# Kernel optimization log

Hardware: AMD Instinct MI355X
Metric: run time of the kernel (lower is better)

## Reference

```python
import jax, jax.numpy as jnp
import numpy as np

EMB = 1024
HEADS = 16
HEAD_DIM = EMB // HEADS  # 64


def setup_inputs() -> dict:
    key = jax.random.key(0)
    ks = jax.random.split(key, 11)
    B, S = 2, 2048
    scale = 1.0 / np.sqrt(EMB)
    inp = {
        "xv": jax.random.normal(ks[0], (B, S, EMB), jnp.float32),
        "xk": jax.random.normal(ks[1], (B, S, EMB), jnp.float32),
        "xq": jax.random.normal(ks[2], (B, S, EMB), jnp.float32),
        "Wq": jax.random.normal(ks[3], (EMB, EMB), jnp.float32) * scale,
        "bq": jax.random.normal(ks[4], (EMB,), jnp.float32) * 0.01,
        "Wk": jax.random.normal(ks[5], (EMB, EMB), jnp.float32) * scale,
        "bk": jax.random.normal(ks[6], (EMB,), jnp.float32) * 0.01,
        "Wv": jax.random.normal(ks[7], (EMB, EMB), jnp.float32) * scale,
        "bv": jax.random.normal(ks[8], (EMB,), jnp.float32) * 0.01,
        "Wo": jax.random.normal(ks[9], (EMB, EMB), jnp.float32) * scale,
        "bo": jax.random.normal(ks[10], (EMB,), jnp.float32) * 0.01,
    }
    return inp


def reference(xv, xk, xq, Wq, bq, Wk, bk, Wv, bv, Wo, bo):
    B, S, E = xq.shape
    H, D = HEADS, HEAD_DIM
    # projections (x @ W + b), split into heads: [B,S,H,D]
    Q = (xq @ Wq + bq).reshape(B, S, H, D)
    K = (xk @ Wk + bk).reshape(B, S, H, D)
    V = (xv @ Wv + bv).reshape(B, S, H, D)
    # scaled dot-product attention per head (vectorized over heads)
    scores = jnp.einsum("bqhd,bkhd->bhqk", Q, K) / jnp.sqrt(jnp.float32(D))
    attn = jax.nn.softmax(scores, axis=-1)
    ctx = jnp.einsum("bhqk,bkhd->bqhd", attn, V).reshape(B, S, E)
    return ctx @ Wo + bo
```

## Files before the change

### kernel.cpp

```cpp
#include <hip/hip_runtime.h>
#include <hip/hip_bf16.h>

typedef __hip_bfloat16 bf16;
typedef __attribute__((ext_vector_type(8))) short short8;
typedef __attribute__((ext_vector_type(4))) short short4v;
typedef __attribute__((ext_vector_type(4))) float floatx4;

#define MFMA16 __builtin_amdgcn_mfma_f32_16x16x32_bf16
#define BARRIER __builtin_amdgcn_s_barrier
#define SCHEDB0() __builtin_amdgcn_sched_barrier(0)
#define SETPRIO __builtin_amdgcn_s_setprio


__device__ __forceinline__ void gl16(const void* g, void* l) {
    __builtin_amdgcn_global_load_lds(
        (const __attribute__((address_space(1))) void*)g,
        (__attribute__((address_space(3))) void*)l, 16, 0, 0);
}

__global__ __launch_bounds__(256) void wtrans_k(const float* __restrict__ w0,
                                                const float* __restrict__ w1,
                                                const float* __restrict__ w2,
                                                const float* __restrict__ w3,
                                                bf16* __restrict__ dst) {
    const float* srcs[4] = {w0, w1, w2, w3};
    const float* src = srcs[blockIdx.z];
    bf16* d = dst + (size_t)blockIdx.z * 1024 * 1024;
    __shared__ float t[32][33];
    int tx = threadIdx.x, ty = threadIdx.y;
    int x0 = blockIdx.x * 32, y0 = blockIdx.y * 32;
#pragma unroll
    for (int i = 0; i < 4; i++)
        t[ty + i * 8][tx] = src[(size_t)(y0 + ty + i * 8) * 1024 + x0 + tx];
    __syncthreads();
#pragma unroll
    for (int i = 0; i < 4; i++)
        d[(size_t)(x0 + ty + i * 8) * 1024 + y0 + tx] =
            __float2bfloat16(t[tx][ty + i * 8]);
}

__global__ __launch_bounds__(256) void xcast_k(const float* __restrict__ x0,
                                               const float* __restrict__ x1,
                                               const float* __restrict__ x2,
                                               bf16* __restrict__ dst) {
    const float* srcs[3] = {x0, x1, x2};
    const float* src = srcs[blockIdx.y];
    bf16* d = dst + (size_t)blockIdx.y * (4096 * 1024);
    size_t i = (size_t)blockIdx.x * 256 + threadIdx.x;
    const float4* s4 = (const float4*)src + i * 2;
    float4 a = s4[0], b = s4[1];
    union { __hip_bfloat162 h2[4]; short8 s; } pk;
    pk.h2[0] = __float22bfloat162_rn(make_float2(a.x, a.y));
    pk.h2[1] = __float22bfloat162_rn(make_float2(a.z, a.w));
    pk.h2[2] = __float22bfloat162_rn(make_float2(b.x, b.y));
    pk.h2[3] = __float22bfloat162_rn(make_float2(b.z, b.w));
    *(short8*)&d[i * 8] = pk.s;
}

__global__ __launch_bounds__(256) void qkv_k(const bf16* __restrict__ xb,
                                             const bf16* __restrict__ wt,
                                             const float* __restrict__ bq,
                                             const float* __restrict__ bk,
                                             const float* __restrict__ bv,
                                             bf16* __restrict__ Qw,
                                             bf16* __restrict__ Kw,
                                             bf16* __restrict__ Vt) {
    __shared__ __align__(16) bf16 lA[3][128 * 32];
    __shared__ __align__(16) bf16 lB[3][128 * 32];
    int z = blockIdx.z;
    const bf16* A = xb + (size_t)z * (4096 * 1024);
    const bf16* Bt = wt + (size_t)z * (1024 * 1024);
    const float* bias = (z == 0) ? bq : (z == 1) ? bk : bv;
    int m0 = blockIdx.x * 128, n0 = blockIdx.y * 128;
    int tid = threadIdx.x, wave = tid >> 6, lane = tid & 63;
    int lm = lane & 15, quad = lane >> 4;
    int wm = wave >> 1, wn = wave & 1;
    int swb = quad ^ ((lm >> 1) & 3);

    floatx4 acc[4][4];
#pragma unroll
    for (int i = 0; i < 4; i++)
#pragma unroll
        for (int j = 0; j < 4; j++) acc[i][j] = (floatx4){0.f, 0.f, 0.f, 0.f};

    auto stage = [&](int bufi, int kt) {
#pragma unroll
        for (int q2 = 0; q2 < 2; q2++) {
            int slot0 = wave * 128 + q2 * 64;
            int r = (slot0 + lane) >> 2;
            int c = (lane & 3) ^ ((r >> 1) & 3);
            gl16(&A[(size_t)(m0 + r) * 1024 + kt * 32 + c * 8],
                 &lA[bufi][slot0 * 8]);
            gl16(&Bt[(size_t)(n0 + r) * 1024 + kt * 32 + c * 8],
                 &lB[bufi][slot0 * 8]);
        }
    };

    auto compute = [&](int cur) {
        short8 af[4], bfr[4];
#pragma unroll
        for (int ms = 0; ms < 4; ms++) {
            int r = wm * 64 + ms * 16 + lm;
            af[ms] = *(const short8*)&lA[cur][(r * 4 + swb) * 8];
        }
#pragma unroll
        for (int ns = 0; ns < 4; ns++) {
            int r = wn * 64 + ns * 16 + lm;
            bfr[ns] = *(const short8*)&lB[cur][(r * 4 + swb) * 8];
        }
        SETPRIO(1);
#pragma unroll
        for (int ms = 0; ms < 4; ms++)
#pragma unroll
            for (int ns = 0; ns < 4; ns++)
                acc[ms][ns] = MFMA16(af[ms], bfr[ns], acc[ms][ns], 0, 0, 0);
        SETPRIO(0);
    };

    stage(0, 0);
    stage(1, 1);
    for (int kt = 0; kt < 32; kt++) {
        int cur = kt % 3;
        BARRIER();
        if (kt < 30) {
            stage((kt + 2) % 3, kt + 2);
            asm volatile("s_waitcnt vmcnt(8)" ::: "memory");
        } else if (kt == 30) {
            asm volatile("s_waitcnt vmcnt(4)" ::: "memory");
        } else {
            asm volatile("s_waitcnt vmcnt(0)" ::: "memory");
        }
        BARRIER();
        SCHEDB0();
        compute(cur);
    }

    bf16* dstQK = (z == 0) ? Qw : Kw;
    float scale = (z == 0) ? 0.125f * 1.44269504f : 1.0f;
#pragma unroll
    for (int ms = 0; ms < 4; ms++) {
        int rowb = m0 + wm * 64 + ms * 16 + quad * 4;
        int bb = rowb >> 11, s0 = rowb & 2047;
#pragma unroll
        for (int ns = 0; ns < 4; ns++) {
            int col = n0 + wn * 64 + ns * 16 + lm;
            float bvv = bias[col];
            int hh = col >> 6, d = col & 63;
            if (z < 2) {
#pragma unroll
                for (int rr = 0; rr < 4; rr++) {
                    float v = (acc[ms][ns][rr] + bvv) * scale;
                    dstQK[((((size_t)bb * 16 + hh) * 2048 + s0 + rr) << 6) + d] =
                        __float2bfloat16(v);
                }
            } else {
                short4v pk;
#pragma unroll
                for (int rr = 0; rr < 4; rr++) {
                    bf16 h = __float2bfloat16(acc[ms][ns][rr] + bvv);
                    pk[rr] = *(short*)&h;
                }
                *(short4v*)&Vt[((((size_t)bb * 16 + hh) * 64 + d) << 11) + s0] = pk;
            }
        }
    }
}

__global__ __launch_bounds__(256) void outproj_k(const bf16* __restrict__ ctx,
                                                 const bf16* __restrict__ wot,
                                                 const float* __restrict__ bo,
                                                 float* __restrict__ out) {
    __shared__ __align__(16) bf16 lA[2][128 * 32];
    __shared__ __align__(16) bf16 lB[2][64 * 32];
    int m0 = blockIdx.x * 128, n0 = blockIdx.y * 64;
    int tid = threadIdx.x, wave = tid >> 6, lane = tid & 63;
    int lm = lane & 15, quad = lane >> 4;
    int wm = wave >> 1, wn = wave & 1;
    int swb = quad ^ ((lm >> 1) & 3);

    floatx4 acc[4][2];
#pragma unroll
    for (int i = 0; i < 4; i++)
#pragma unroll
        for (int j = 0; j < 2; j++) acc[i][j] = (floatx4){0.f, 0.f, 0.f, 0.f};

    auto stage = [&](int bufi, int kt) {
#pragma unroll
        for (int q2 = 0; q2 < 2; q2++) {
            int slot0 = wave * 128 + q2 * 64;
            int r = (slot0 + lane) >> 2;
            int c = (lane & 3) ^ ((r >> 1) & 3);
            gl16(&ctx[(size_t)(m0 + r) * 1024 + kt * 32 + c * 8],
                 &lA[bufi][slot0 * 8]);
        }
        {
            int slot0 = wave * 64;
            int r = (slot0 + lane) >> 2;
            int c = (lane & 3) ^ ((r >> 1) & 3);
            gl16(&wot[(size_t)(n0 + r) * 1024 + kt * 32 + c * 8],
                 &lB[bufi][slot0 * 8]);
        }
    };

    auto compute = [&](int cur) {
        short8 af[4], bfr[2];
#pragma unroll
        for (int ms = 0; ms < 4; ms++) {
            int r = wm * 64 + ms * 16 + lm;
            af[ms] = *(const short8*)&lA[cur][(r * 4 + swb) * 8];
        }
#pragma unroll
        for (int ns = 0; ns < 2; ns++) {
            int r = wn * 32 + ns * 16 + lm;
            bfr[ns] = *(const short8*)&lB[cur][(r * 4 + swb) * 8];
        }
        SETPRIO(1);
#pragma unroll
        for (int ms = 0; ms < 4; ms++)
#pragma unroll
            for (int ns = 0; ns < 2; ns++)
                acc[ms][ns] = MFMA16(af[ms], bfr[ns], acc[ms][ns], 0, 0, 0);
        SETPRIO(0);
    };

    stage(0, 0);
    for (int kt = 0; kt < 31; kt++) {
        int cur = kt & 1;
        BARRIER();
        stage(cur ^ 1, kt + 1);
        asm volatile("s_waitcnt vmcnt(3)" ::: "memory");
        BARRIER();
        SCHEDB0();
        compute(cur);
    }
    BARRIER();
    asm volatile("s_waitcnt vmcnt(0)" ::: "memory");
    BARRIER();
    SCHEDB0();
    compute(1);

#pragma unroll
    for (int ms = 0; ms < 4; ms++) {
        int rowb = m0 + wm * 64 + ms * 16 + quad * 4;
#pragma unroll
        for (int ns = 0; ns < 2; ns++) {
            int col = n0 + wn * 32 + ns * 16 + lm;
            float bvv = bo[col];
#pragma unroll
            for (int rr = 0; rr < 4; rr++)
                out[(size_t)(rowb + rr) * 1024 + col] = acc[ms][ns][rr] + bvv;
        }
    }
}

__global__ __launch_bounds__(512, 4) void attn_k(const bf16* __restrict__ Q,
                                                 const bf16* __restrict__ K,
                                                 const bf16* __restrict__ Vt,
                                                 bf16* __restrict__ ctx) {
    __shared__ __align__(16) bf16 lKV[2][2][64 * 64];
    __shared__ float scrL[4][32];
    int bh = blockIdx.x, qt = blockIdx.y;
    int b = bh >> 4, h = bh & 15;
    const bf16* Qh = Q + (size_t)bh * (2048 * 64);
    const bf16* Kh = K + (size_t)bh * (2048 * 64);
    const bf16* Vh = Vt + (size_t)bh * (64 * 2048);
    int tid = threadIdx.x, wave = tid >> 6, lane = tid & 63;
    int lm = lane & 15, quad = lane >> 4;
    int s7 = lm & 7;
    int wq = wave >> 1, wk = wave & 1;

    short8 qf[2][2];
#pragma unroll
    for (int qblk = 0; qblk < 2; qblk++) {
        int qrow = qt * 128 + wq * 32 + qblk * 16 + lm;
        qf[qblk][0] = *(const short8*)&Qh[(size_t)qrow * 64 + quad * 8];
        qf[qblk][1] = *(const short8*)&Qh[(size_t)qrow * 64 + 32 + quad * 8];
    }

    short8 onesf;
#pragma unroll
    for (int i = 0; i < 8; i++) onesf[i] = (short)0x3F80;

    floatx4 o[2][4];
#pragma unroll
    for (int i = 0; i < 2; i++)
#pragma unroll
        for (int j = 0; j < 4; j++) o[i][j] = (floatx4){0.f, 0.f, 0.f, 0.f};
    floatx4 accL[2];
#pragma unroll
    for (int i = 0; i < 2; i++) accL[i] = (floatx4){0.f, 0.f, 0.f, 0.f};

    auto stage = [&](int bufi, int kt) {
        int slot0 = wave * 64;
        int r = (slot0 + lane) >> 3;
        int c = (lane & 7) ^ (r & 7);
        gl16(&Kh[(size_t)(kt * 64 + r) * 64 + c * 8], &lKV[0][bufi][slot0 * 8]);
        gl16(&Vh[(size_t)r * 2048 + kt * 64 + c * 8], &lKV[1][bufi][slot0 * 8]);
    };

    auto compute = [&](int cur) {
        short8 kf[2][2];
#pragma unroll
        for (int ksub = 0; ksub < 2; ksub++) {
            int r = wk * 32 + ksub * 16 + lm;
#pragma unroll
            for (int ds = 0; ds < 2; ds++)
                kf[ksub][ds] = *(const short8*)
                    &lKV[0][cur][(r * 8 + ((ds * 4 + quad) ^ s7)) * 8];
        }
        floatx4 s[2][2];
#pragma unroll
        for (int i = 0; i < 2; i++)
#pragma unroll
            for (int j = 0; j < 2; j++) s[i][j] = (floatx4){0.f, 0.f, 0.f, 0.f};
        SETPRIO(1);
#pragma unroll
        for (int qblk = 0; qblk < 2; qblk++)
#pragma unroll
            for (int ksub = 0; ksub < 2; ksub++) {
                s[qblk][ksub] = MFMA16(kf[ksub][0], qf[qblk][0], s[qblk][ksub], 0, 0, 0);
                s[qblk][ksub] = MFMA16(kf[ksub][1], qf[qblk][1], s[qblk][ksub], 0, 0, 0);
            }
        SETPRIO(0);

        short8 pz[2];
#pragma unroll
        for (int qblk = 0; qblk < 2; qblk++) {
            union { short4v h[2]; short8 s8; } up;
#pragma unroll
            for (int ksub = 0; ksub < 2; ksub++) {
                float p0 = __builtin_amdgcn_exp2f(s[qblk][ksub][0]);
                float p1 = __builtin_amdgcn_exp2f(s[qblk][ksub][1]);
                float p2 = __builtin_amdgcn_exp2f(s[qblk][ksub][2]);
                float p3 = __builtin_amdgcn_exp2f(s[qblk][ksub][3]);
                union { __hip_bfloat162 b2[2]; short4v s4; } c;
                c.b2[0] = __float22bfloat162_rn(make_float2(p0, p1));
                c.b2[1] = __float22bfloat162_rn(make_float2(p2, p3));
                up.h[ksub] = c.s4;
            }
            pz[qblk] = up.s8;
        }

        short8 vfz[4];
#pragma unroll
        for (int dblk = 0; dblk < 4; dblk++) {
            int d = dblk * 16 + lm;
            union { short4v h[2]; short8 s8; } uv;
#pragma unroll
            for (int ksub = 0; ksub < 2; ksub++) {
                int g = 4 * wk + 2 * ksub + (quad >> 1);
                uv.h[ksub] = *(const short4v*)
                    &lKV[1][cur][(d * 8 + (g ^ s7)) * 8 + (quad & 1) * 4];
            }
            vfz[dblk] = uv.s8;
        }

        SETPRIO(1);
#pragma unroll
        for (int qblk = 0; qblk < 2; qblk++) {
            accL[qblk] = MFMA16(pz[qblk], onesf, accL[qblk], 0, 0, 0);
#pragma unroll
            for (int dblk = 0; dblk < 4; dblk++)
                o[qblk][dblk] = MFMA16(pz[qblk], vfz[dblk], o[qblk][dblk], 0, 0, 0);
        }
        SETPRIO(0);
    };

    stage(0, 0);
    for (int kt = 0; kt < 31; kt++) {
        int cur = kt & 1;
        BARRIER();
        stage(cur ^ 1, kt + 1);
        asm volatile("s_waitcnt vmcnt(2)" ::: "memory");
        BARRIER();
        SCHEDB0();
        compute(cur);
    }
    BARRIER();
    asm volatile("s_waitcnt vmcnt(0)" ::: "memory");
    BARRIER();
    SCHEDB0();
    compute(1);

    __syncthreads();
    float* scrO = (float*)&lKV[0][0][0];
    if (wk == 1) {
#pragma unroll
        for (int qblk = 0; qblk < 2; qblk++) {
#pragma unroll
            for (int dblk = 0; dblk < 4; dblk++)
#pragma unroll
                for (int rr = 0; rr < 4; rr++)
                    scrO[wq * 2048 + (qblk * 16 + quad * 4 + rr) * 64 +
                         dblk * 16 + lm] = o[qblk][dblk][rr];
#pragma unroll
            for (int rr = 0; rr < 4; rr++)
                scrL[wq][qblk * 16 + quad * 4 + rr] = accL[qblk][rr];
        }
    }
    __syncthreads();
    if (wk == 0) {
#pragma unroll
        for (int qblk = 0; qblk < 2; qblk++) {
            float inv[4];
#pragma unroll
            for (int rr = 0; rr < 4; rr++)
                inv[rr] = 1.f / (accL[qblk][rr] +
                                 scrL[wq][qblk * 16 + quad * 4 + rr]);
#pragma unroll
            for (int dblk = 0; dblk < 4; dblk++) {
                int e = h * 64 + dblk * 16 + lm;
#pragma unroll
                for (int rr = 0; rr < 4; rr++) {
                    int srow = qt * 128 + wq * 32 + qblk * 16 + quad * 4 + rr;
                    float of = o[qblk][dblk][rr] +
                               scrO[wq * 2048 + (qblk * 16 + quad * 4 + rr) * 64 +
                                    dblk * 16 + lm];
                    ctx[(size_t)(b * 2048 + srow) * 1024 + e] =
                        __float2bfloat16(of * inv[rr]);
                }
            }
        }
    }
}

extern "C" void kernel_launch(void* const* d_in, const int* in_sizes, int n_in,
                              void* d_out, int out_size, void* d_ws, size_t ws_size,
                              hipStream_t stream) {
    const float* xv = (const float*)d_in[0];
    const float* xk = (const float*)d_in[1];
    const float* xq = (const float*)d_in[2];
    const float* Wq = (const float*)d_in[3];
    const float* bq = (const float*)d_in[4];
    const float* Wk = (const float*)d_in[5];
    const float* bk = (const float*)d_in[6];
    const float* Wv = (const float*)d_in[7];
    const float* bv = (const float*)d_in[8];
    const float* Wo = (const float*)d_in[9];
    const float* bo = (const float*)d_in[10];
    float* out = (float*)d_out;
    bf16* ws = (bf16*)d_ws;

    const size_t MB1 = 1024 * 1024;
    bf16* wt  = ws;
    bf16* Qw  = ws + 4 * MB1;
    bf16* Kw  = ws + 8 * MB1;
    bf16* Vt  = ws + 12 * MB1;
    bf16* ctx = ws + 16 * MB1;
    bf16* xb  = ws + 20 * MB1;

    hipLaunchKernelGGL(wtrans_k, dim3(32, 32, 4), dim3(32, 8), 0, stream,
                       Wq, Wk, Wv, Wo, wt);

    hipLaunchKernelGGL(xcast_k, dim3(2048, 3), dim3(256), 0, stream,
                       xq, xk, xv, xb);

    hipLaunchKernelGGL(qkv_k, dim3(32, 8, 3), dim3(256), 0, stream,
                       xb, wt, bq, bk, bv, Qw, Kw, Vt);

    hipLaunchKernelGGL(attn_k, dim3(32, 16), dim3(512), 0, stream, Qw, Kw, Vt, ctx);

    hipLaunchKernelGGL(outproj_k, dim3(32, 16), dim3(256), 0, stream,
                       ctx, wt + 3 * MB1, bo, out);
}
```

Before: 208.9 us.

## Double attention KV tile to 128 keys and merge prep kernels into one launch

The attention kernel now stages 128 keys per iteration instead of 64 into separate K and V LDS buffers. This halves the loop trip count and the barrier/wait overhead per key, and doubles the MFMA work between syncs. It costs more LDS per block (64KB total), which may cut occupancy below the launch_bounds target of 4 blocks. Separately, the weight-transpose and input-cast kernels are merged into one launch to save a kernel launch and its tail.

```diff
diff --git a/kernel.cpp b/kernel.cpp
--- a/kernel.cpp
+++ b/kernel.cpp
@@ -18,43 +18,48 @@
         (__attribute__((address_space(3))) void*)l, 16, 0, 0);
 }
 
-__global__ __launch_bounds__(256) void wtrans_k(const float* __restrict__ w0,
-                                                const float* __restrict__ w1,
-                                                const float* __restrict__ w2,
-                                                const float* __restrict__ w3,
-                                                bf16* __restrict__ dst) {
-    const float* srcs[4] = {w0, w1, w2, w3};
-    const float* src = srcs[blockIdx.z];
-    bf16* d = dst + (size_t)blockIdx.z * 1024 * 1024;
-    __shared__ float t[32][33];
-    int tx = threadIdx.x, ty = threadIdx.y;
-    int x0 = blockIdx.x * 32, y0 = blockIdx.y * 32;
-#pragma unroll
-    for (int i = 0; i < 4; i++)
-        t[ty + i * 8][tx] = src[(size_t)(y0 + ty + i * 8) * 1024 + x0 + tx];
-    __syncthreads();
-#pragma unroll
-    for (int i = 0; i < 4; i++)
-        d[(size_t)(x0 + ty + i * 8) * 1024 + y0 + tx] =
-            __float2bfloat16(t[tx][ty + i * 8]);
-}
-
-__global__ __launch_bounds__(256) void xcast_k(const float* __restrict__ x0,
-                                               const float* __restrict__ x1,
-                                               const float* __restrict__ x2,
-                                               bf16* __restrict__ dst) {
-    const float* srcs[3] = {x0, x1, x2};
-    const float* src = srcs[blockIdx.y];
-    bf16* d = dst + (size_t)blockIdx.y * (4096 * 1024);
-    size_t i = (size_t)blockIdx.x * 256 + threadIdx.x;
-    const float4* s4 = (const float4*)src + i * 2;
-    float4 a = s4[0], b = s4[1];
-    union { __hip_bfloat162 h2[4]; short8 s; } pk;
-    pk.h2[0] = __float22bfloat162_rn(make_float2(a.x, a.y));
-    pk.h2[1] = __float22bfloat162_rn(make_float2(a.z, a.w));
-    pk.h2[2] = __float22bfloat162_rn(make_float2(b.x, b.y));
-    pk.h2[3] = __float22bfloat162_rn(make_float2(b.z, b.w));
-    *(short8*)&d[i * 8] = pk.s;
+__global__ __launch_bounds__(256) void prep_k(const float* __restrict__ w0,
+                                              const float* __restrict__ w1,
+                                              const float* __restrict__ w2,
+                                              const float* __restrict__ w3,
+                                              bf16* __restrict__ wdst,
+                                              const float* __restrict__ x0,
+                                              const float* __restrict__ x1,
+                                              const float* __restrict__ x2,
+                                              bf16* __restrict__ xdst) {
+    int bid = blockIdx.x, tid = threadIdx.x;
+    if (bid < 4096) {
+        const float* srcs[4] = {w0, w1, w2, w3};
+        int z = bid >> 10, by = (bid >> 5) & 31, bx = bid & 31;
+        const float* src = srcs[z];
+        bf16* d = wdst + (size_t)z * 1024 * 1024;
+        __shared__ float t[32][33];
+        int tx = tid & 31, ty = tid >> 5;
+        int x0c = bx * 32, y0 = by * 32;
+#pragma unroll
+        for (int i = 0; i < 4; i++)
+            t[ty + i * 8][tx] = src[(size_t)(y0 + ty + i * 8) * 1024 + x0c + tx];
+        __syncthreads();
+#pragma unroll
+        for (int i = 0; i < 4; i++)
+            d[(size_t)(x0c + ty + i * 8) * 1024 + y0 + tx] =
+                __float2bfloat16(t[tx][ty + i * 8]);
+    } else {
+        int ib = bid - 4096;
+        int zc = ib >> 11, blk = ib & 2047;
+        const float* srcs[3] = {x0, x1, x2};
+        const float* src = srcs[zc];
+        bf16* d = xdst + (size_t)zc * (4096 * 1024);
+        size_t i = (size_t)blk * 256 + tid;
+        const float4* s4 = (const float4*)src + i * 2;
+        float4 a = s4[0], b = s4[1];
+        union { __hip_bfloat162 h2[4]; short8 s; } pk;
+        pk.h2[0] = __float22bfloat162_rn(make_float2(a.x, a.y));
+        pk.h2[1] = __float22bfloat162_rn(make_float2(a.z, a.w));
+        pk.h2[2] = __float22bfloat162_rn(make_float2(b.x, b.y));
+        pk.h2[3] = __float22bfloat162_rn(make_float2(b.z, b.w));
+        *(short8*)&d[i * 8] = pk.s;
+    }
 }
 
 __global__ __launch_bounds__(256) void qkv_k(const bf16* __restrict__ xb,
@@ -257,7 +262,8 @@
                                                  const bf16* __restrict__ K,
                                                  const bf16* __restrict__ Vt,
                                                  bf16* __restrict__ ctx) {
-    __shared__ __align__(16) bf16 lKV[2][2][64 * 64];
+    __shared__ __align__(16) bf16 lK[2][128 * 64];
+    __shared__ __align__(16) bf16 lV[2][64 * 128];
     __shared__ float scrL[4][32];
     int bh = blockIdx.x, qt = blockIdx.y;
     int b = bh >> 4, h = bh & 15;
@@ -291,87 +297,106 @@
     for (int i = 0; i < 2; i++) accL[i] = (floatx4){0.f, 0.f, 0.f, 0.f};
 
     auto stage = [&](int bufi, int kt) {
-        int slot0 = wave * 64;
-        int r = (slot0 + lane) >> 3;
-        int c = (lane & 7) ^ (r & 7);
-        gl16(&Kh[(size_t)(kt * 64 + r) * 64 + c * 8], &lKV[0][bufi][slot0 * 8]);
-        gl16(&Vh[(size_t)r * 2048 + kt * 64 + c * 8], &lKV[1][bufi][slot0 * 8]);
+#pragma unroll
+        for (int q2 = 0; q2 < 2; q2++) {
+            int slot0 = wave * 128 + q2 * 64;
+            int r = (slot0 + lane) >> 3;
+            int c = (lane & 7) ^ (r & 7);
+            gl16(&Kh[(size_t)(kt * 128 + r) * 64 + c * 8], &lK[bufi][slot0 * 8]);
+        }
+#pragma unroll
+        for (int q2 = 0; q2 < 2; q2++) {
+            int slot0 = wave * 128 + q2 * 64;
+            int s = slot0 + lane;
+            int r = s >> 4, cl = s & 15;
+            int c = cl ^ (r & 7);
+            gl16(&Vh[(size_t)r * 2048 + kt * 128 + c * 8], &lV[bufi][slot0 * 8]);
+        }
     };
 
     auto compute = [&](int cur) {
-        short8 kf[2][2];
-#pragma unroll
-        for (int ksub = 0; ksub < 2; ksub++) {
-            int r = wk * 32 + ksub * 16 + lm;
+        short8 kf[4][2];
+#pragma unroll
+        for (int ksub = 0; ksub < 4; ksub++) {
+            int r = wk * 64 + ksub * 16 + lm;
 #pragma unroll
             for (int ds = 0; ds < 2; ds++)
                 kf[ksub][ds] = *(const short8*)
-                    &lKV[0][cur][(r * 8 + ((ds * 4 + quad) ^ s7)) * 8];
-        }
-        floatx4 s[2][2];
+                    &lK[cur][(r * 8 + ((ds * 4 + quad) ^ s7)) * 8];
+        }
+        floatx4 s[2][4];
 #pragma unroll
         for (int i = 0; i < 2; i++)
 #pragma unroll
-            for (int j = 0; j < 2; j++) s[i][j] = (floatx4){0.f, 0.f, 0.f, 0.f};
+            for (int j = 0; j < 4; j++) s[i][j] = (floatx4){0.f, 0.f, 0.f, 0.f};
         SETPRIO(1);
 #pragma unroll
         for (int qblk = 0; qblk < 2; qblk++)
 #pragma unroll
-            for (int ksub = 0; ksub < 2; ksub++) {
+            for (int ksub = 0; ksub < 4; ksub++) {
                 s[qblk][ksub] = MFMA16(kf[ksub][0], qf[qblk][0], s[qblk][ksub], 0, 0, 0);
                 s[qblk][ksub] = MFMA16(kf[ksub][1], qf[qblk][1], s[qblk][ksub], 0, 0, 0);
             }
         SETPRIO(0);
 
-        short8 pz[2];
+        short8 pz[2][2];
+#pragma unroll
+        for (int qblk = 0; qblk < 2; qblk++)
+#pragma unroll
+            for (int ks = 0; ks < 2; ks++) {
+                union { short4v h[2]; short8 s8; } up;
+#pragma unroll
+                for (int j = 0; j < 2; j++) {
+                    int ksub = ks * 2 + j;
+                    float p0 = __builtin_amdgcn_exp2f(s[qblk][ksub][0]);
+                    float p1 = __builtin_amdgcn_exp2f(s[qblk][ksub][1]);
+                    float p2 = __builtin_amdgcn_exp2f(s[qblk][ksub][2]);
+                    float p3 = __builtin_amdgcn_exp2f(s[qblk][ksub][3]);
+                    union { __hip_bfloat162 b2[2]; short4v s4; } c;
+                    c.b2[0] = __float22bfloat162_rn(make_float2(p0, p1));
+                    c.b2[1] = __float22bfloat162_rn(make_float2(p2, p3));
+                    up.h[j] = c.s4;
+                }
+                pz[qblk][ks] = up.s8;
+            }
+
+        short8 vfz[2][4];
+#pragma unroll
+        for (int ks = 0; ks < 2; ks++)
+#pragma unroll
+            for (int dblk = 0; dblk < 4; dblk++) {
+                int d = dblk * 16 + lm;
+                union { short4v h[2]; short8 s8; } uv;
+#pragma unroll
+                for (int j = 0; j < 2; j++) {
+                    int c = wk * 8 + (ks * 2 + j) * 2 + (quad >> 1);
+                    uv.h[j] = *(const short4v*)
+                        &lV[cur][(d * 16 + (c ^ s7)) * 8 + (quad & 1) * 4];
+                }
+                vfz[ks][dblk] = uv.s8;
+            }
+
+        SETPRIO(1);
 #pragma unroll
         for (int qblk = 0; qblk < 2; qblk++) {
-            union { short4v h[2]; short8 s8; } up;
-#pragma unroll
-            for (int ksub = 0; ksub < 2; ksub++) {
-                float p0 = __builtin_amdgcn_exp2f(s[qblk][ksub][0]);
-                float p1 = __builtin_amdgcn_exp2f(s[qblk][ksub][1]);
-                float p2 = __builtin_amdgcn_exp2f(s[qblk][ksub][2]);
-                float p3 = __builtin_amdgcn_exp2f(s[qblk][ksub][3]);
-                union { __hip_bfloat162 b2[2]; short4v s4; } c;
-                c.b2[0] = __float22bfloat162_rn(make_float2(p0, p1));
-                c.b2[1] = __float22bfloat162_rn(make_float2(p2, p3));
-                up.h[ksub] = c.s4;
-            }
-            pz[qblk] = up.s8;
-        }
-
-        short8 vfz[4];
-#pragma unroll
-        for (int dblk = 0; dblk < 4; dblk++) {
-            int d = dblk * 16 + lm;
-            union { short4v h[2]; short8 s8; } uv;
-#pragma unroll
-            for (int ksub = 0; ksub < 2; ksub++) {
-                int g = 4 * wk + 2 * ksub + (quad >> 1);
-                uv.h[ksub] = *(const short4v*)
-                    &lKV[1][cur][(d * 8 + (g ^ s7)) * 8 + (quad & 1) * 4];
-            }
-            vfz[dblk] = uv.s8;
-        }
-
-        SETPRIO(1);
-#pragma unroll
-        for (int qblk = 0; qblk < 2; qblk++) {
-            accL[qblk] = MFMA16(pz[qblk], onesf, accL[qblk], 0, 0, 0);
-#pragma unroll
-            for (int dblk = 0; dblk < 4; dblk++)
-                o[qblk][dblk] = MFMA16(pz[qblk], vfz[dblk], o[qblk][dblk], 0, 0, 0);
+#pragma unroll
+            for (int ks = 0; ks < 2; ks++) {
+                accL[qblk] = MFMA16(pz[qblk][ks], onesf, accL[qblk], 0, 0, 0);
+#pragma unroll
+                for (int dblk = 0; dblk < 4; dblk++)
+                    o[qblk][dblk] = MFMA16(pz[qblk][ks], vfz[ks][dblk],
+                                           o[qblk][dblk], 0, 0, 0);
+            }
         }
         SETPRIO(0);
     };
 
     stage(0, 0);
-    for (int kt = 0; kt < 31; kt++) {
+    for (int kt = 0; kt < 15; kt++) {
         int cur = kt & 1;
         BARRIER();
         stage(cur ^ 1, kt + 1);
-        asm volatile("s_waitcnt vmcnt(2)" ::: "memory");
+        asm volatile("s_waitcnt vmcnt(4)" ::: "memory");
         BARRIER();
         SCHEDB0();
         compute(cur);
@@ -383,7 +408,7 @@
     compute(1);
 
     __syncthreads();
-    float* scrO = (float*)&lKV[0][0][0];
+    float* scrO = (float*)&lK[0][0];
     if (wk == 1) {
 #pragma unroll
         for (int qblk = 0; qblk < 2; qblk++) {
@@ -449,11 +474,8 @@
     bf16* ctx = ws + 16 * MB1;
     bf16* xb  = ws + 20 * MB1;
 
-    hipLaunchKernelGGL(wtrans_k, dim3(32, 32, 4), dim3(32, 8), 0, stream,
-                       Wq, Wk, Wv, Wo, wt);
-
-    hipLaunchKernelGGL(xcast_k, dim3(2048, 3), dim3(256), 0, stream,
-                       xq, xk, xv, xb);
+    hipLaunchKernelGGL(prep_k, dim3(10240), dim3(256), 0, stream,
+                       Wq, Wk, Wv, Wo, wt, xq, xk, xv, xb);
 
     hipLaunchKernelGGL(qkv_k, dim3(32, 8, 3), dim3(256), 0, stream,
                        xb, wt, bq, bk, bv, Qw, Kw, Vt);
```

Measured after the change: 244.2 us. +16.9%, slower.

## Fuse fp32-to-bf16 input cast into QKV GEMM and shrink outproj tiles

Applied to the files above, without the earlier changes.

Removes the separate xcast kernel and instead loads fp32 activations directly in the QKV GEMM, converting to bf16 in registers before writing to LDS, with the pipeline reduced from three to two buffers. This saves writing and rereading the 24 MB bf16 copy of the inputs, at the cost of register-staged loads that cannot use direct global-to-LDS transfer and a shallower prefetch. Separately, the output projection tile shrinks from 128x64 to 64x64, doubling the grid for better CU occupancy at the cost of more redundant weight reads.

```diff
diff --git a/kernel.cpp b/kernel.cpp
--- a/kernel.cpp
+++ b/kernel.cpp
@@ -39,25 +39,9 @@
             __float2bfloat16(t[tx][ty + i * 8]);
 }
 
-__global__ __launch_bounds__(256) void xcast_k(const float* __restrict__ x0,
-                                               const float* __restrict__ x1,
-                                               const float* __restrict__ x2,
-                                               bf16* __restrict__ dst) {
-    const float* srcs[3] = {x0, x1, x2};
-    const float* src = srcs[blockIdx.y];
-    bf16* d = dst + (size_t)blockIdx.y * (4096 * 1024);
-    size_t i = (size_t)blockIdx.x * 256 + threadIdx.x;
-    const float4* s4 = (const float4*)src + i * 2;
-    float4 a = s4[0], b = s4[1];
-    union { __hip_bfloat162 h2[4]; short8 s; } pk;
-    pk.h2[0] = __float22bfloat162_rn(make_float2(a.x, a.y));
-    pk.h2[1] = __float22bfloat162_rn(make_float2(a.z, a.w));
-    pk.h2[2] = __float22bfloat162_rn(make_float2(b.x, b.y));
-    pk.h2[3] = __float22bfloat162_rn(make_float2(b.z, b.w));
-    *(short8*)&d[i * 8] = pk.s;
-}
-
-__global__ __launch_bounds__(256) void qkv_k(const bf16* __restrict__ xb,
+__global__ __launch_bounds__(256) void qkv_k(const float* __restrict__ xq,
+                                             const float* __restrict__ xk,
+                                             const float* __restrict__ xv,
                                              const bf16* __restrict__ wt,
                                              const float* __restrict__ bq,
                                              const float* __restrict__ bk,
@@ -65,10 +49,10 @@
                                              bf16* __restrict__ Qw,
                                              bf16* __restrict__ Kw,
                                              bf16* __restrict__ Vt) {
-    __shared__ __align__(16) bf16 lA[3][128 * 32];
-    __shared__ __align__(16) bf16 lB[3][128 * 32];
+    __shared__ __align__(16) bf16 lA[2][128 * 32];
+    __shared__ __align__(16) bf16 lB[2][128 * 32];
     int z = blockIdx.z;
-    const bf16* A = xb + (size_t)z * (4096 * 1024);
+    const float* A = (z == 0) ? xq : (z == 1) ? xk : xv;
     const bf16* Bt = wt + (size_t)z * (1024 * 1024);
     const float* bias = (z == 0) ? bq : (z == 1) ? bk : bv;
     int m0 = blockIdx.x * 128, n0 = blockIdx.y * 128;
@@ -77,22 +61,46 @@
     int wm = wave >> 1, wn = wave & 1;
     int swb = quad ^ ((lm >> 1) & 3);
 
+    int sA0 = wave * 128 + lane, sA1 = wave * 128 + 64 + lane;
+
     floatx4 acc[4][4];
 #pragma unroll
     for (int i = 0; i < 4; i++)
 #pragma unroll
         for (int j = 0; j < 4; j++) acc[i][j] = (floatx4){0.f, 0.f, 0.f, 0.f};
 
-    auto stage = [&](int bufi, int kt) {
+    float4 ar[2][2];
+    auto issueA = [&](int kt) {
+#pragma unroll
+        for (int i = 0; i < 2; i++) {
+            int s = i ? sA1 : sA0;
+            int r = s >> 2, j = s & 3;
+            int c = j ^ ((r >> 1) & 3);
+            const float4* p =
+                (const float4*)&A[(size_t)(m0 + r) * 1024 + kt * 32 + c * 8];
+            ar[i][0] = p[0];
+            ar[i][1] = p[1];
+        }
+    };
+    auto issueB = [&](int bufi, int kt) {
 #pragma unroll
         for (int q2 = 0; q2 < 2; q2++) {
             int slot0 = wave * 128 + q2 * 64;
             int r = (slot0 + lane) >> 2;
             int c = (lane & 3) ^ ((r >> 1) & 3);
-            gl16(&A[(size_t)(m0 + r) * 1024 + kt * 32 + c * 8],
-                 &lA[bufi][slot0 * 8]);
             gl16(&Bt[(size_t)(n0 + r) * 1024 + kt * 32 + c * 8],
                  &lB[bufi][slot0 * 8]);
+        }
+    };
+    auto writeA = [&](int bufi) {
+#pragma unroll
+        for (int i = 0; i < 2; i++) {
+            union { __hip_bfloat162 h2[4]; short8 s8; } pk;
+            pk.h2[0] = __float22bfloat162_rn(make_float2(ar[i][0].x, ar[i][0].y));
+            pk.h2[1] = __float22bfloat162_rn(make_float2(ar[i][0].z, ar[i][0].w));
+            pk.h2[2] = __float22bfloat162_rn(make_float2(ar[i][1].x, ar[i][1].y));
+            pk.h2[3] = __float22bfloat162_rn(make_float2(ar[i][1].z, ar[i][1].w));
+            *(short8*)&lA[bufi][(i ? sA1 : sA0) * 8] = pk.s8;
         }
     };
 
@@ -117,16 +125,23 @@
         SETPRIO(0);
     };
 
-    stage(0, 0);
-    stage(1, 1);
+    issueA(0);
+    SCHEDB0();
+    issueB(0, 0);
+    SCHEDB0();
+    writeA(0);
+    asm volatile("s_waitcnt lgkmcnt(0)" ::: "memory");
+
     for (int kt = 0; kt < 32; kt++) {
-        int cur = kt % 3;
-        BARRIER();
-        if (kt < 30) {
-            stage((kt + 2) % 3, kt + 2);
-            asm volatile("s_waitcnt vmcnt(8)" ::: "memory");
-        } else if (kt == 30) {
-            asm volatile("s_waitcnt vmcnt(4)" ::: "memory");
+        int cur = kt & 1;
+        BARRIER();
+        if (kt < 31) {
+            issueA(kt + 1);
+            SCHEDB0();
+            issueB(cur ^ 1, kt + 1);
+            SCHEDB0();
+            writeA(cur ^ 1);
+            asm volatile("s_waitcnt lgkmcnt(0)" ::: "memory");
         } else {
             asm volatile("s_waitcnt vmcnt(0)" ::: "memory");
         }
@@ -170,43 +185,35 @@
                                                  const bf16* __restrict__ wot,
                                                  const float* __restrict__ bo,
                                                  float* __restrict__ out) {
-    __shared__ __align__(16) bf16 lA[2][128 * 32];
+    __shared__ __align__(16) bf16 lA[2][64 * 32];
     __shared__ __align__(16) bf16 lB[2][64 * 32];
-    int m0 = blockIdx.x * 128, n0 = blockIdx.y * 64;
+    int m0 = blockIdx.x * 64, n0 = blockIdx.y * 64;
     int tid = threadIdx.x, wave = tid >> 6, lane = tid & 63;
     int lm = lane & 15, quad = lane >> 4;
     int wm = wave >> 1, wn = wave & 1;
     int swb = quad ^ ((lm >> 1) & 3);
 
-    floatx4 acc[4][2];
-#pragma unroll
-    for (int i = 0; i < 4; i++)
+    floatx4 acc[2][2];
+#pragma unroll
+    for (int i = 0; i < 2; i++)
 #pragma unroll
         for (int j = 0; j < 2; j++) acc[i][j] = (floatx4){0.f, 0.f, 0.f, 0.f};
 
     auto stage = [&](int bufi, int kt) {
-#pragma unroll
-        for (int q2 = 0; q2 < 2; q2++) {
-            int slot0 = wave * 128 + q2 * 64;
-            int r = (slot0 + lane) >> 2;
-            int c = (lane & 3) ^ ((r >> 1) & 3);
-            gl16(&ctx[(size_t)(m0 + r) * 1024 + kt * 32 + c * 8],
-                 &lA[bufi][slot0 * 8]);
-        }
-        {
-            int slot0 = wave * 64;
-            int r = (slot0 + lane) >> 2;
-            int c = (lane & 3) ^ ((r >> 1) & 3);
-            gl16(&wot[(size_t)(n0 + r) * 1024 + kt * 32 + c * 8],
-                 &lB[bufi][slot0 * 8]);
-        }
+        int slot0 = wave * 64;
+        int r = (slot0 + lane) >> 2;
+        int c = (lane & 3) ^ ((r >> 1) & 3);
+        gl16(&ctx[(size_t)(m0 + r) * 1024 + kt * 32 + c * 8],
+             &lA[bufi][slot0 * 8]);
+        gl16(&wot[(size_t)(n0 + r) * 1024 + kt * 32 + c * 8],
+             &lB[bufi][slot0 * 8]);
     };
 
     auto compute = [&](int cur) {
-        short8 af[4], bfr[2];
-#pragma unroll
-        for (int ms = 0; ms < 4; ms++) {
-            int r = wm * 64 + ms * 16 + lm;
+        short8 af[2], bfr[2];
+#pragma unroll
+        for (int ms = 0; ms < 2; ms++) {
+            int r = wm * 32 + ms * 16 + lm;
             af[ms] = *(const short8*)&lA[cur][(r * 4 + swb) * 8];
         }
 #pragma unroll
@@ -216,7 +223,7 @@
         }
         SETPRIO(1);
 #pragma unroll
-        for (int ms = 0; ms < 4; ms++)
+        for (int ms = 0; ms < 2; ms++)
 #pragma unroll
             for (int ns = 0; ns < 2; ns++)
                 acc[ms][ns] = MFMA16(af[ms], bfr[ns], acc[ms][ns], 0, 0, 0);
@@ -228,7 +235,7 @@
         int cur = kt & 1;
         BARRIER();
         stage(cur ^ 1, kt + 1);
-        asm volatile("s_waitcnt vmcnt(3)" ::: "memory");
+        asm volatile("s_waitcnt vmcnt(2)" ::: "memory");
         BARRIER();
         SCHEDB0();
         compute(cur);
@@ -240,8 +247,8 @@
     compute(1);
 
 #pragma unroll
-    for (int ms = 0; ms < 4; ms++) {
-        int rowb = m0 + wm * 64 + ms * 16 + quad * 4;
+    for (int ms = 0; ms < 2; ms++) {
+        int rowb = m0 + wm * 32 + ms * 16 + quad * 4;
 #pragma unroll
         for (int ns = 0; ns < 2; ns++) {
             int col = n0 + wn * 32 + ns * 16 + lm;
@@ -447,19 +454,15 @@
     bf16* Kw  = ws + 8 * MB1;
     bf16* Vt  = ws + 12 * MB1;
     bf16* ctx = ws + 16 * MB1;
-    bf16* xb  = ws + 20 * MB1;
 
     hipLaunchKernelGGL(wtrans_k, dim3(32, 32, 4), dim3(32, 8), 0, stream,
                        Wq, Wk, Wv, Wo, wt);
 
-    hipLaunchKernelGGL(xcast_k, dim3(2048, 3), dim3(256), 0, stream,
-                       xq, xk, xv, xb);
-
     hipLaunchKernelGGL(qkv_k, dim3(32, 8, 3), dim3(256), 0, stream,
-                       xb, wt, bq, bk, bv, Qw, Kw, Vt);
+                       xq, xk, xv, wt, bq, bk, bv, Qw, Kw, Vt);
 
     hipLaunchKernelGGL(attn_k, dim3(32, 16), dim3(512), 0, stream, Qw, Kw, Vt, ctx);
 
-    hipLaunchKernelGGL(outproj_k, dim3(32, 16), dim3(256), 0, stream,
+    hipLaunchKernelGGL(outproj_k, dim3(64, 16), dim3(256), 0, stream,
                        ctx, wt + 3 * MB1, bo, out);
 }
```

Result: slower. 221.3 us (+5.9%).
